# Optimization experiments

Measured on AMD Instinct MI355X. Metric: run time of the kernel, lower is better.

The kernel has to match this reference:

```python
import jax, jax.numpy as jnp
import numpy as np

B, T, D, H, TW = 4, 2048, 2048, 8, 4
DH = D // H


def setup_inputs() -> dict:
    key = jax.random.key(0)
    ks = jax.random.split(key, 16)
    s = lambda k, shape, std: jax.random.normal(k, shape, dtype=jnp.float32) * std
    inp = {
        "x": jax.random.normal(ks[0], (B, T, D), dtype=jnp.float32),
        "segment_pos": jnp.tile(jnp.arange(T, dtype=jnp.int32), (B, 1)),
        # linear_y / linear_x: width -> lru_width, std = 1/sqrt(width)
        "Wy": s(ks[1], (D, D), (1.0 / D) ** 0.5),
        "by": jnp.zeros((D,), jnp.float32),
        "Wx": s(ks[2], (D, D), (1.0 / D) ** 0.5),
        "bx": jnp.zeros((D,), jnp.float32),
        # depthwise causal conv: [temporal_width, lru_width]
        "conv_w": s(ks[3], (TW, D), (1.0 / TW) ** 0.5),
        "conv_b": jnp.zeros((D,), jnp.float32),
        # RG-LRU block-diagonal gates: [H, D/H, D/H]
        "gx_w": s(ks[4], (H, DH, DH), (1.0 / DH) ** 0.5),
        "gx_b": jnp.zeros((H, DH), jnp.float32),
        "ga_w": s(ks[5], (H, DH, DH), (1.0 / DH) ** 0.5),
        "ga_b": jnp.zeros((H, DH), jnp.float32),
        # a_param: softplus(a_param) > 0 controls decay rate
        "a_param": jnp.log(jnp.exp(jax.random.uniform(ks[6], (D,), minval=0.3, maxval=0.9)) - 1.0 + 1e-6),
        # linear_out: lru_width -> width, std = 1/sqrt(lru_width)
        "Wout": s(ks[7], (D, D), (1.0 / D) ** 0.5),
        "bout": jnp.zeros((D,), jnp.float32),
    }
    return inp


def _causal_conv1d(x, w, b, segment_pos):
    # depthwise causal conv over time; contributions from other segments masked
    t = x.shape[1]
    acc = jnp.zeros_like(x)
    for i in range(TW):
        shift = TW - 1 - i  # input at t - shift, weighted by w[i]
        xs = x if shift == 0 else jnp.pad(x, ((0, 0), (shift, 0), (0, 0)))[:, :t]
        mask = (segment_pos >= shift)[..., None].astype(x.dtype)
        acc = acc + xs * mask * w[i]
    return acc + b


def _rg_lru(x, segment_pos, gx_w, gx_b, ga_w, ga_b, a_param):
    b, t, d = x.shape
    xr = x.reshape(b, t, H, DH)
    gate_x = jax.nn.sigmoid(jnp.einsum("bthi,hij->bthj", xr, gx_w) + gx_b).reshape(b, t, d)
    gate_a = jax.nn.sigmoid(jnp.einsum("bthi,hij->bthj", xr, ga_w) + ga_b).reshape(b, t, d)
    log_a = -8.0 * gate_a * jax.nn.softplus(a_param)  # [B,T,D]
    a = jnp.exp(log_a)
    reset = (segment_pos == 0)[..., None]  # [B,T,1]
    multiplier = jnp.sqrt(jnp.maximum(1.0 - jnp.exp(2.0 * log_a), 0.0))
    multiplier = jnp.where(reset, 1.0, multiplier)
    normed = x * gate_x * multiplier
    a_scan = jnp.where(reset, 0.0, a)

    def step(h, inputs):
        a_t, x_t = inputs
        h = a_t * h + x_t
        return h, h

    h0 = jnp.zeros((b, d), x.dtype)
    _, ys = jax.lax.scan(step, h0, (a_scan.transpose(1, 0, 2), normed.transpose(1, 0, 2)))
    return ys.transpose(1, 0, 2)


def reference(x, segment_pos, Wy, by, Wx, bx, conv_w, conv_b, gx_w, gx_b, ga_w, ga_b, a_param, Wout, bout):
    y = jax.nn.gelu(x @ Wy.T + by, approximate=True)
    x_proj = x @ Wx.T + bx
    x_conv = _causal_conv1d(x_proj, conv_w, conv_b, segment_pos)
    x_lru = _rg_lru(x_conv, segment_pos, gx_w, gx_b, ga_w, ga_b, a_param)
    out = (x_lru * y) @ Wout.T + bout
    return out
```

## Files before the change

kernel.cpp:

```cpp
#include <hip/hip_runtime.h>
#include <cstdint>
#include <cstddef>

typedef __bf16 bf16;
typedef __bf16 bf16x8 __attribute__((ext_vector_type(8)));
typedef float f32x4 __attribute__((ext_vector_type(4)));

#define BDIM 4
#define TDIM 2048
#define DDIM 2048
#define HDIM 8
#define DHD 256
#define MTOT 8192
#define NCHUNK 64
#define LCHUNK 32

__device__ __forceinline__ void stage16(const bf16* g, bf16* l) {
  __builtin_amdgcn_global_load_lds(
      (const __attribute__((address_space(1))) void*)g,
      (__attribute__((address_space(3))) void*)l, 16, 0, 0);
}

#define BARX() __builtin_amdgcn_s_barrier()
#define SCHB() __builtin_amdgcn_sched_barrier(0)
#define WAITVM(N) asm volatile("s_waitcnt vmcnt(" #N ")")

__device__ __forceinline__ float sigmoid_f(float x) {
  return __fdividef(1.f, 1.f + __expf(-x));
}
__device__ __forceinline__ float gelu_tanh(float v) {
  float u = 0.7978845608028654f * (v + 0.044715f * v * v * v);
  u = fminf(fmaxf(u, -15.f), 15.f);
  float t = __expf(2.f * u);
  return 0.5f * v * (1.f + __fdividef(t - 1.f, t + 1.f));
}
__device__ __forceinline__ float softplus_f(float x) {
  return __logf(1.f + __expf(x));
}

__global__ __launch_bounds__(256) void f2b(const float* __restrict__ src,
                                           bf16* __restrict__ dst) {
  size_t i = ((size_t)blockIdx.x * 256 + threadIdx.x) * 8;
  const float4 a = *(const float4*)(src + i);
  const float4 b = *(const float4*)(src + i + 4);
  bf16x8 r;
  r[0] = (bf16)a.x; r[1] = (bf16)a.y; r[2] = (bf16)a.z; r[3] = (bf16)a.w;
  r[4] = (bf16)b.x; r[5] = (bf16)b.y; r[6] = (bf16)b.z; r[7] = (bf16)b.w;
  *(bf16x8*)(dst + i) = r;
}

template <typename TO, int EPI>
__global__ __launch_bounds__(512, 2) void gemm256(
    const bf16* __restrict__ A, const bf16* __restrict__ Bm,
    const float* __restrict__ bias, TO* __restrict__ C,
    int K, int lda, int ldb, int ldc) {
  const int gx = gridDim.x, gy = gridDim.y;
  const int nwg = gx * gy;
  const int did = blockIdx.x + gx * blockIdx.y;
  const int cpx = nwg >> 3;
  const int lid = (did & 7) * cpx + (did >> 3);
  const int n0 = (lid % gx) * 256;
  const int m0 = (lid / gx) * 256;

  __shared__ bf16 sA0[256 * 64];
  __shared__ bf16 sA1[256 * 64];
  __shared__ bf16 sB0[256 * 64];
  __shared__ bf16 sB1[256 * 64];
  const int tid = threadIdx.x;
  const int lane = tid & 63;
  const int wid = tid >> 6;
  const int wr = wid >> 2;
  const int wc = wid & 3;
  const int quad = lane >> 4;
  const int l15 = lane & 15;

  const int sr = tid >> 3;
  const int ks8 = ((tid & 7) ^ (sr & 7)) << 3;
  const bf16* Ag = A + (size_t)(m0 + sr) * lda + ks8;
  const bf16* Bg = Bm + (size_t)(n0 + sr) * ldb + ks8;

  const int swz0 = ((quad) ^ (l15 & 7)) << 3;
  const int swz1 = ((4 + quad) ^ (l15 & 7)) << 3;

  f32x4 acc[8][4];
#pragma unroll
  for (int i = 0; i < 8; ++i)
#pragma unroll
    for (int j = 0; j < 4; ++j)
#pragma unroll
      for (int r = 0; r < 4; ++r) acc[i][j][r] = 0.f;

  const int NT = K >> 6;

#define STG_A(ARR, H, TK)                                                     \
  do {                                                                        \
    _Pragma("unroll") for (int j_ = 0; j_ < 2; ++j_) {                        \
      const int c_ = (H) * 2 + j_;                                            \
      stage16(Ag + (size_t)(c_ * 64) * lda + (size_t)(TK) * 64,               \
              &ARR[(c_ * 64 + wid * 8) * 64]);                                \
    }                                                                         \
  } while (0)
#define STG_B(ARR, H, TK)                                                     \
  do {                                                                        \
    _Pragma("unroll") for (int j_ = 0; j_ < 2; ++j_) {                        \
      const int c_ = (H) * 2 + j_;                                            \
      stage16(Bg + (size_t)(c_ * 64) * ldb + (size_t)(TK) * 64,               \
              &ARR[(c_ * 64 + wid * 8) * 64]);                                \
    }                                                                         \
  } while (0)

  bf16x8 aq0[4][2], aq1[4][2], b0[2][2], b1[2][2];

#define RDA(DST, MH, ARR)                                                     \
  do {                                                                        \
    _Pragma("unroll") for (int mi_ = 0; mi_ < 4; ++mi_) {                     \
      const int arow_ = wr * 128 + (MH) * 64 + mi_ * 16 + l15;                \
      DST[mi_][0] = *(const bf16x8*)(&ARR[arow_ * 64] + swz0);                \
      DST[mi_][1] = *(const bf16x8*)(&ARR[arow_ * 64] + swz1);                \
    }                                                                         \
  } while (0)
#define RDB(DST, NH, ARR)                                                     \
  do {                                                                        \
    _Pragma("unroll") for (int ni_ = 0; ni_ < 2; ++ni_) {                     \
      const int brow_ = wc * 64 + (NH) * 32 + ni_ * 16 + l15;                 \
      DST[ni_][0] = *(const bf16x8*)(&ARR[brow_ * 64] + swz0);                \
      DST[ni_][1] = *(const bf16x8*)(&ARR[brow_ * 64] + swz1);                \
    }                                                                         \
  } while (0)
#define MFMAQ(MH, NH, AA, BB)                                                 \
  do {                                                                        \
    __builtin_amdgcn_s_setprio(1);                                            \
    _Pragma("unroll") for (int mi_ = 0; mi_ < 4; ++mi_)                       \
        _Pragma("unroll") for (int ni_ = 0; ni_ < 2; ++ni_) {                 \
      acc[(MH)*4 + mi_][(NH)*2 + ni_] = __builtin_amdgcn_mfma_f32_16x16x32_bf16( \
          AA[mi_][0], BB[ni_][0], acc[(MH)*4 + mi_][(NH)*2 + ni_], 0, 0, 0);  \
      acc[(MH)*4 + mi_][(NH)*2 + ni_] = __builtin_amdgcn_mfma_f32_16x16x32_bf16( \
          AA[mi_][1], BB[ni_][1], acc[(MH)*4 + mi_][(NH)*2 + ni_], 0, 0, 0);  \
    }                                                                         \
    __builtin_amdgcn_s_setprio(0);                                            \
  } while (0)

#define TILE(SAs, SBs, SAo, SBo, T)                                           \
  do {                                                                        \
    const int tn_ = ((T) + 1 < NT) ? (T) + 1 : NT - 1;                        \
    const int tnn_ = ((T) + 2 < NT) ? (T) + 2 : NT - 1;                       \
                                                                     \
    WAITVM(4);                                                                \
    SCHB();                                                                   \
    STG_B(SBo, 1, tn_);                                                       \
    RDB(b1, 1, SBs);                                                          \
    MFMAQ(0, 0, aq0, b0);                                                     \
    BARX();                                                                   \
                                                                     \
    STG_A(SAo, 1, tn_);                                                       \
    RDA(aq1, 1, SAs);                                                         \
    MFMAQ(0, 1, aq0, b1);                                                     \
    BARX();                                                                   \
                                                                     \
    STG_B(SBs, 0, tnn_);                                                      \
    MFMAQ(1, 0, aq1, b0);                                                     \
    BARX();                                                                   \
                                                                     \
    WAITVM(6);                                                                \
    SCHB();                                                                   \
    STG_A(SAs, 0, tnn_);                                                      \
    RDA(aq0, 0, SAo);                                                         \
    RDB(b0, 0, SBo);                                                          \
    MFMAQ(1, 1, aq1, b1);                                                     \
    BARX();                                                                   \
  } while (0)

  STG_B(sB0, 0, 0); STG_A(sA0, 0, 0);
  STG_B(sB0, 1, 0); STG_A(sA0, 1, 0);
  STG_B(sB1, 0, 1); STG_A(sA1, 0, 1);
  WAITVM(8);
  SCHB();
  BARX();
  RDA(aq0, 0, sA0);
  RDB(b0, 0, sB0);

  for (int t = 0; t < NT; t += 2) {
    TILE(sA0, sB0, sA1, sB1, t);
    TILE(sA1, sB1, sA0, sB0, t + 1);
  }
  WAITVM(0);

#undef STG_A
#undef STG_B
#undef RDA
#undef RDB
#undef MFMAQ
#undef TILE

  float bv[4];
#pragma unroll
  for (int nn = 0; nn < 4; ++nn) bv[nn] = bias[n0 + wc * 64 + nn * 16 + l15];
#pragma unroll
  for (int mm = 0; mm < 8; ++mm) {
#pragma unroll
    for (int r = 0; r < 4; ++r) {
      const int m = m0 + wr * 128 + mm * 16 + quad * 4 + r;
      TO* Crow = C + (size_t)m * ldc + n0 + wc * 64 + l15;
#pragma unroll
      for (int nn = 0; nn < 4; ++nn) {
        float v = acc[mm][nn][r] + bv[nn];
        if (EPI == 1) v = gelu_tanh(v);
        Crow[nn * 16] = (TO)v;
      }
    }
  }
}

__global__ __launch_bounds__(256) void gate_gemm(
    const bf16* __restrict__ xconv,
    const bf16* __restrict__ gxT, const bf16* __restrict__ gaT,
    bf16* __restrict__ gxr, bf16* __restrict__ gar) {
  const int h = blockIdx.z >> 1;
  const int g = blockIdx.z & 1;
  const bf16* A = xconv + h * DHD;
  const bf16* Bm = (g ? gaT : gxT) + (size_t)h * DHD * DHD;
  bf16* C = (g ? gar : gxr) + h * DHD;
  const int n0 = blockIdx.x * 128;
  const int m0 = blockIdx.y * 128;
  __shared__ bf16 As[128 * 32];
  __shared__ bf16 Bs[128 * 32];
  const int tid = threadIdx.x;
  const int lane = tid & 63;
  const int wid = tid >> 6;
  const int waveM = wid >> 1, waveN = wid & 1;
  const int quad = lane >> 4;
  const int l15 = lane & 15;
  const int srow = lane >> 2;
  const int scol = (lane & 3) * 8;

  f32x4 acc[4][4];
#pragma unroll
  for (int i = 0; i < 4; ++i)
#pragma unroll
    for (int j = 0; j < 4; ++j)
#pragma unroll
      for (int r = 0; r < 4; ++r) acc[i][j][r] = 0.f;

  for (int k0 = 0; k0 < DHD; k0 += 32) {
    if (k0) __syncthreads();
#pragma unroll
    for (int cc = 0; cc < 2; ++cc) {
      const int q = wid * 2 + cc;
      const int row = q * 16 + srow;
      stage16(A + (size_t)(m0 + row) * DDIM + k0 + scol, As + q * 512);
      stage16(Bm + (size_t)(n0 + row) * DHD + k0 + scol, Bs + q * 512);
    }
    __syncthreads();
    bf16x8 af[4], bfr[4];
#pragma unroll
    for (int i = 0; i < 4; ++i) {
      af[i]  = *(const bf16x8*)&As[(waveM * 64 + i * 16 + l15) * 32 + quad * 8];
      bfr[i] = *(const bf16x8*)&Bs[(waveN * 64 + i * 16 + l15) * 32 + quad * 8];
    }
#pragma unroll
    for (int i = 0; i < 4; ++i)
#pragma unroll
      for (int j = 0; j < 4; ++j)
        acc[i][j] = __builtin_amdgcn_mfma_f32_16x16x32_bf16(af[i], bfr[j], acc[i][j], 0, 0, 0);
  }

#pragma unroll
  for (int j = 0; j < 4; ++j) {
    const int n = n0 + waveN * 64 + j * 16 + l15;
#pragma unroll
    for (int i = 0; i < 4; ++i) {
#pragma unroll
      for (int r = 0; r < 4; ++r) {
        const int m = m0 + waveM * 64 + i * 16 + quad * 4 + r;
        C[(size_t)m * DDIM + n] = (bf16)acc[i][j][r];
      }
    }
  }
}

__global__ __launch_bounds__(256) void conv_kernel(
    const bf16* __restrict__ xp, const float* __restrict__ cw,
    const float* __restrict__ cb, const int* __restrict__ segp,
    bf16* __restrict__ xc) {
  int v = blockIdx.x * 256 + threadIdx.x;
  int dv = v & (DDIM / 8 - 1);
  int m = v >> 8;
  int d0 = dv * 8;
  int t = m & (TDIM - 1);
  int sp = segp[m];
  float acc[8];
#pragma unroll
  for (int j = 0; j < 8; ++j) acc[j] = cb[d0 + j];
#pragma unroll
  for (int i = 0; i < 4; ++i) {
    int shift = 3 - i;
    if (t >= shift && sp >= shift) {
      bf16x8 xv = *(const bf16x8*)&xp[(size_t)(m - shift) * DDIM + d0];
#pragma unroll
      for (int j = 0; j < 8; ++j) acc[j] = fmaf((float)xv[j], cw[i * DDIM + d0 + j], acc[j]);
    }
  }
  bf16x8 o;
#pragma unroll
  for (int j = 0; j < 8; ++j) o[j] = (bf16)acc[j];
  *(bf16x8*)&xc[(size_t)m * DDIM + d0] = o;
}

__global__ __launch_bounds__(256) void transpose_gates(
    const float* __restrict__ gxw, const float* __restrict__ gaw,
    bf16* __restrict__ gxT, bf16* __restrict__ gaT) {
  __shared__ bf16 tile[32][33];
  int zz = blockIdx.z;
  int h = zz >> 1;
  const float* src = (zz & 1) ? gaw : gxw;
  bf16* dst = (zz & 1) ? gaT : gxT;
  int j0 = blockIdx.x * 32;
  int i0 = blockIdx.y * 32;
  int r = threadIdx.x >> 5;
  int c = threadIdx.x & 31;
  for (int rr = r; rr < 32; rr += 8)
    tile[rr][c] = (bf16)src[(size_t)(h * DHD + i0 + rr) * DHD + j0 + c];
  __syncthreads();
  for (int rr = r; rr < 32; rr += 8)
    dst[(size_t)(h * DHD + j0 + rr) * DHD + i0 + c] = tile[c][rr];
}

__device__ __forceinline__ void lru_elem(float pgx, float pga, float xc,
                                         float spv, bool reset,
                                         float& a, float& nr) {
  const float gx = sigmoid_f(pgx);
  const float ga = sigmoid_f(pga);
  const float la = -8.f * ga * spv;
  a = reset ? 0.f : __expf(la);
  const float mult = reset ? 1.f : sqrtf(fmaxf(1.f - __expf(2.f * la), 0.f));
  nr = xc * gx * mult;
}

__global__ __launch_bounds__(256) void scan_phase1(
    const bf16* __restrict__ gxr, const bf16* __restrict__ gar,
    const bf16* __restrict__ xconv,
    const float* __restrict__ gxb, const float* __restrict__ gab,
    const float* __restrict__ apar, const int* __restrict__ segp,
    float* __restrict__ chA, float* __restrict__ chH) {
  int idx = blockIdx.x * 256 + threadIdx.x;
  int d = idx & (DDIM - 1);
  int c = (idx >> 11) & (NCHUNK - 1);
  int b = idx >> 17;
  const float gxbv = gxb[d], gabv = gab[d];
  const float spv = softplus_f(apar[d]);
  const int mrow = b * TDIM + c * LCHUNK;
  size_t base = (size_t)mrow * DDIM + d;
  float A = 1.f, hh = 0.f;
  for (int i = 0; i < LCHUNK; ++i) {
    size_t o = base + (size_t)i * DDIM;
    float a, nr;
    lru_elem((float)gxr[o] + gxbv, (float)gar[o] + gabv, (float)xconv[o],
             spv, segp[mrow + i] == 0, a, nr);
    hh = fmaf(a, hh, nr);
    A *= a;
  }
  int ci = (b * NCHUNK + c) * DDIM + d;
  chA[ci] = A;
  chH[ci] = hh;
}

__global__ __launch_bounds__(256) void scan_phase2(
    const float* __restrict__ chA, const float* __restrict__ chH,
    float* __restrict__ hst) {
  int idx = blockIdx.x * 256 + threadIdx.x;
  int d = idx & (DDIM - 1);
  int b = idx >> 11;
  float s = 0.f;
  for (int c = 0; c < NCHUNK; ++c) {
    int ci = (b * NCHUNK + c) * DDIM + d;
    hst[ci] = s;
    s = fmaf(chA[ci], s, chH[ci]);
  }
}

__global__ __launch_bounds__(256) void scan_phase3(
    const bf16* __restrict__ gxr, const bf16* __restrict__ gar,
    const bf16* __restrict__ xconv,
    const float* __restrict__ gxb, const float* __restrict__ gab,
    const float* __restrict__ apar, const int* __restrict__ segp,
    const float* __restrict__ hst, bf16* __restrict__ yz) {
  int idx = blockIdx.x * 256 + threadIdx.x;
  int d = idx & (DDIM - 1);
  int c = (idx >> 11) & (NCHUNK - 1);
  int b = idx >> 17;
  const float gxbv = gxb[d], gabv = gab[d];
  const float spv = softplus_f(apar[d]);
  const int mrow = b * TDIM + c * LCHUNK;
  size_t base = (size_t)mrow * DDIM + d;
  float hh = hst[(b * NCHUNK + c) * DDIM + d];
  for (int i = 0; i < LCHUNK; ++i) {
    size_t o = base + (size_t)i * DDIM;
    float a, nr;
    lru_elem((float)gxr[o] + gxbv, (float)gar[o] + gabv, (float)xconv[o],
             spv, segp[mrow + i] == 0, a, nr);
    hh = fmaf(a, hh, nr);
    yz[o] = (bf16)(hh * (float)yz[o]);
  }
}

extern "C" void kernel_launch(void* const* d_in, const int* in_sizes, int n_in,
                              void* d_out, int out_size, void* d_ws, size_t ws_size,
                              hipStream_t stream) {
  const float* x    = (const float*)d_in[0];
  const int*   segp = (const int*)d_in[1];
  const float* Wy   = (const float*)d_in[2];
  const float* by   = (const float*)d_in[3];
  const float* Wx   = (const float*)d_in[4];
  const float* bx   = (const float*)d_in[5];
  const float* cw   = (const float*)d_in[6];
  const float* cb   = (const float*)d_in[7];
  const float* gxw  = (const float*)d_in[8];
  const float* gxb  = (const float*)d_in[9];
  const float* gaw  = (const float*)d_in[10];
  const float* gab  = (const float*)d_in[11];
  const float* apar = (const float*)d_in[12];
  const float* Wout = (const float*)d_in[13];
  const float* bout = (const float*)d_in[14];

  const size_t MD = (size_t)MTOT * DDIM;
  const size_t WD = (size_t)DDIM * DDIM;
  bf16* xb    = (bf16*)d_out;
  bf16* xproj = (bf16*)((char*)d_out + MD * 2);
  bf16* xconv = xb;
  bf16* gxr   = xproj;

  char* ws = (char*)d_ws;
  bf16*  gar = (bf16*)ws;
  bf16*  W1  = (bf16*)(ws + MD * 2);
  bf16*  WB1 = (bf16*)(ws + 2 * MD * 2);
  bf16*  WB2 = (bf16*)(ws + 2 * MD * 2 + WD * 2);
  char*  tail = ws + 2 * MD * 2 + 2 * WD * 2;
  const size_t GW = (size_t)HDIM * DHD * DHD * 2;
  const size_t CH = (size_t)BDIM * NCHUNK * DDIM * 4;
  bf16*  gxT = (bf16*)tail;
  bf16*  gaT = (bf16*)(tail + GW);
  float* chA = (float*)(tail + 2 * GW);
  float* chH = (float*)(tail + 2 * GW + CH);
  float* hst = (float*)(tail + 2 * GW + 2 * CH);

  dim3 blk(256);
  f2b<<<dim3(MD / 2048), blk, 0, stream>>>(x, xb);
  f2b<<<dim3(WD / 2048), blk, 0, stream>>>(Wx, WB1);
  f2b<<<dim3(WD / 2048), blk, 0, stream>>>(Wy, WB2);
  transpose_gates<<<dim3(8, 8, 16), blk, 0, stream>>>(gxw, gaw, gxT, gaT);

  gemm256<bf16, 0><<<dim3(8, 32), dim3(512), 0, stream>>>(xb, WB1, bx, xproj, DDIM, DDIM, DDIM, DDIM);
  gemm256<bf16, 1><<<dim3(8, 32), dim3(512), 0, stream>>>(xb, WB2, by, W1, DDIM, DDIM, DDIM, DDIM);

  conv_kernel<<<dim3(MTOT * (DDIM / 8) / 256), blk, 0, stream>>>(xproj, cw, cb, segp, xconv);

  gate_gemm<<<dim3(2, 64, 16), blk, 0, stream>>>(xconv, gxT, gaT, gxr, gar);

  scan_phase1<<<dim3(BDIM * NCHUNK * DDIM / 256), blk, 0, stream>>>(
      gxr, gar, xconv, gxb, gab, apar, segp, chA, chH);
  scan_phase2<<<dim3(BDIM * DDIM / 256), blk, 0, stream>>>(chA, chH, hst);
  scan_phase3<<<dim3(BDIM * NCHUNK * DDIM / 256), blk, 0, stream>>>(
      gxr, gar, xconv, gxb, gab, apar, segp, hst, W1);

  f2b<<<dim3(WD / 2048), blk, 0, stream>>>(Wout, WB1);
  gemm256<float, 0><<<dim3(8, 32), dim3(512), 0, stream>>>(W1, WB1, bout, (float*)d_out, DDIM, DDIM, DDIM, DDIM);
}
```

Baseline: 410.2 us.

## Add batched 128-tile GEMM for input projections and vectorize scan kernels

Adds a 128x128-tile GEMM kernel that computes the x and y input projections in a single launch, using blockIdx.z to select the weight, bias and output, and remaps workgroups for locality. The 256-tile kernel stays in use for the output projection, and its final-iteration LDS prefetch is now skipped. The scan phase-1 and phase-3 kernels each process 8 channels per thread with 16-byte vector loads and stores instead of scalar bf16 accesses. The goals are to cut launches, improve wave occupancy on the projection GEMMs, and raise memory efficiency in the scan. The cost is smaller tiles with less reuse per tile and more registers per thread in the scan.

```diff
diff --git a/kernel.cpp b/kernel.cpp
--- a/kernel.cpp
+++ b/kernel.cpp
@@ -163,9 +163,11 @@
                                                                      \
     WAITVM(6);                                                                \
     SCHB();                                                                   \
+    if (T + 1 < NT) {                                                         \
+      RDA(aq0, 0, SAo);                                                       \
+      RDB(b0, 0, SBo);                                                        \
+    }                                                                         \
     STG_A(SAs, 0, tnn_);                                                      \
-    RDA(aq0, 0, SAo);                                                         \
-    RDB(b0, 0, SBo);                                                          \
     MFMAQ(1, 1, aq1, b1);                                                     \
     BARX();                                                                   \
   } while (0)
@@ -200,6 +202,157 @@
 #pragma unroll
     for (int r = 0; r < 4; ++r) {
       const int m = m0 + wr * 128 + mm * 16 + quad * 4 + r;
+      TO* Crow = C + (size_t)m * ldc + n0 + wc * 64 + l15;
+#pragma unroll
+      for (int nn = 0; nn < 4; ++nn) {
+        float v = acc[mm][nn][r] + bv[nn];
+        if (EPI == 1) v = gelu_tanh(v);
+        Crow[nn * 16] = (TO)v;
+      }
+    }
+  }
+}
+
+template <typename TO>
+__global__ __launch_bounds__(256, 2) void gemm128(
+    const bf16* __restrict__ A,
+    const bf16* __restrict__ B0m, const bf16* __restrict__ B1m,
+    const float* __restrict__ bias0, const float* __restrict__ bias1,
+    TO* __restrict__ C0, TO* __restrict__ C1, int epi1,
+    int K, int lda, int ldb, int ldc) {
+  const bf16* Bm = blockIdx.z ? B1m : B0m;
+  const float* bias = blockIdx.z ? bias1 : bias0;
+  TO* C = blockIdx.z ? C1 : C0;
+  const int EPI = blockIdx.z ? epi1 : 0;
+
+  const int gx = gridDim.x, gy = gridDim.y;
+  const int nwg = gx * gy;
+  const int did = blockIdx.x + gx * blockIdx.y;
+  const int cpx = nwg >> 3;
+  const int lid = (did & 7) * cpx + (did >> 3);
+  const int n0 = (lid % gx) * 128;
+  const int m0 = (lid / gx) * 128;
+
+  __shared__ bf16 sA0[128 * 64];
+  __shared__ bf16 sA1[128 * 64];
+  __shared__ bf16 sB0[128 * 64];
+  __shared__ bf16 sB1[128 * 64];
+  const int tid = threadIdx.x;
+  const int lane = tid & 63;
+  const int wid = tid >> 6;
+  const int wr = wid >> 1;
+  const int wc = wid & 1;
+  const int quad = lane >> 4;
+  const int l15 = lane & 15;
+
+  const int sr = tid >> 3;
+  const int ks8 = ((tid & 7) ^ (sr & 7)) << 3;
+  const bf16* Ag = A + (size_t)(m0 + sr) * lda + ks8;
+  const bf16* Bg = Bm + (size_t)(n0 + sr) * ldb + ks8;
+
+  const int swz0 = ((quad) ^ (l15 & 7)) << 3;
+  const int swz1 = ((4 + quad) ^ (l15 & 7)) << 3;
+
+  f32x4 acc[4][4];
+#pragma unroll
+  for (int i = 0; i < 4; ++i)
+#pragma unroll
+    for (int j = 0; j < 4; ++j)
+#pragma unroll
+      for (int r = 0; r < 4; ++r) acc[i][j][r] = 0.f;
+
+  const int NT = K >> 6;
+
+#define STG_A(ARR, TK)                                                        \
+  do {                                                                        \
+    _Pragma("unroll") for (int c_ = 0; c_ < 4; ++c_)                          \
+        stage16(Ag + (size_t)(c_ * 32) * lda + (size_t)(TK) * 64,             \
+                &ARR[(c_ * 32 + wid * 8) * 64]);                              \
+  } while (0)
+#define STG_B(ARR, TK)                                                        \
+  do {                                                                        \
+    _Pragma("unroll") for (int c_ = 0; c_ < 4; ++c_)                          \
+        stage16(Bg + (size_t)(c_ * 32) * ldb + (size_t)(TK) * 64,             \
+                &ARR[(c_ * 32 + wid * 8) * 64]);                              \
+  } while (0)
+
+  bf16x8 af[4][2], b0[2][2], b1[2][2];
+
+#define RDA(ARR)                                                              \
+  do {                                                                        \
+    _Pragma("unroll") for (int mi_ = 0; mi_ < 4; ++mi_) {                     \
+      const int arow_ = wr * 64 + mi_ * 16 + l15;                             \
+      af[mi_][0] = *(const bf16x8*)(&ARR[arow_ * 64] + swz0);                 \
+      af[mi_][1] = *(const bf16x8*)(&ARR[arow_ * 64] + swz1);                 \
+    }                                                                         \
+  } while (0)
+#define RDB(DST, NH, ARR)                                                     \
+  do {                                                                        \
+    _Pragma("unroll") for (int ni_ = 0; ni_ < 2; ++ni_) {                     \
+      const int brow_ = wc * 64 + (NH) * 32 + ni_ * 16 + l15;                 \
+      DST[ni_][0] = *(const bf16x8*)(&ARR[brow_ * 64] + swz0);                \
+      DST[ni_][1] = *(const bf16x8*)(&ARR[brow_ * 64] + swz1);                \
+    }                                                                         \
+  } while (0)
+#define MFMAQ(NH, BB)                                                         \
+  do {                                                                        \
+    __builtin_amdgcn_s_setprio(1);                                            \
+    _Pragma("unroll") for (int mi_ = 0; mi_ < 4; ++mi_)                       \
+        _Pragma("unroll") for (int ni_ = 0; ni_ < 2; ++ni_) {                 \
+      acc[mi_][(NH)*2 + ni_] = __builtin_amdgcn_mfma_f32_16x16x32_bf16(       \
+          af[mi_][0], BB[ni_][0], acc[mi_][(NH)*2 + ni_], 0, 0, 0);           \
+      acc[mi_][(NH)*2 + ni_] = __builtin_amdgcn_mfma_f32_16x16x32_bf16(       \
+          af[mi_][1], BB[ni_][1], acc[mi_][(NH)*2 + ni_], 0, 0, 0);           \
+    }                                                                         \
+    __builtin_amdgcn_s_setprio(0);                                            \
+  } while (0)
+
+#define TILE(SAs, SBs, SAo, SBo, T)                                           \
+  do {                                                                        \
+    const int tn_ = ((T) + 1 < NT) ? (T) + 1 : NT - 1;                        \
+    const int tnn_ = ((T) + 2 < NT) ? (T) + 2 : NT - 1;                       \
+                                                                     \
+    RDA(SAs);                                                                 \
+    RDB(b0, 0, SBs);                                                          \
+    STG_B(SBo, tn_);                                                          \
+    MFMAQ(0, b0);                                                             \
+    BARX();                                                                   \
+                                                                     \
+    RDB(b1, 1, SBs);                                                          \
+    STG_A(SAs, tnn_);                                                         \
+    MFMAQ(1, b1);                                                             \
+    WAITVM(4);                                                                \
+    BARX();                                                                   \
+  } while (0)
+
+  const int t1 = (NT > 1) ? 1 : 0;
+  STG_B(sB0, 0); STG_A(sA0, 0);
+  STG_B(sB1, t1); STG_A(sA1, t1);
+  WAITVM(4);
+  SCHB();
+  BARX();
+
+  for (int t = 0; t < NT; t += 2) {
+    TILE(sA0, sB0, sA1, sB1, t);
+    TILE(sA1, sB1, sA0, sB0, t + 1);
+  }
+  WAITVM(0);
+
+#undef STG_A
+#undef STG_B
+#undef RDA
+#undef RDB
+#undef MFMAQ
+#undef TILE
+
+  float bv[4];
+#pragma unroll
+  for (int nn = 0; nn < 4; ++nn) bv[nn] = bias[n0 + wc * 64 + nn * 16 + l15];
+#pragma unroll
+  for (int mm = 0; mm < 4; ++mm) {
+#pragma unroll
+    for (int r = 0; r < 4; ++r) {
+      const int m = m0 + wr * 64 + mm * 16 + quad * 4 + r;
       TO* Crow = C + (size_t)m * ldc + n0 + wc * 64 + l15;
 #pragma unroll
       for (int nn = 0; nn < 4; ++nn) {
@@ -343,25 +496,45 @@
     const float* __restrict__ apar, const int* __restrict__ segp,
     float* __restrict__ chA, float* __restrict__ chH) {
   int idx = blockIdx.x * 256 + threadIdx.x;
-  int d = idx & (DDIM - 1);
-  int c = (idx >> 11) & (NCHUNK - 1);
-  int b = idx >> 17;
-  const float gxbv = gxb[d], gabv = gab[d];
-  const float spv = softplus_f(apar[d]);
+  int dv = idx & (DDIM / 8 - 1);
+  int c = (idx >> 8) & (NCHUNK - 1);
+  int b = idx >> 14;
+  int d0 = dv * 8;
+  float gxbv[8], gabv[8], spv[8];
+  const float4 gx0 = *(const float4*)(gxb + d0), gx1 = *(const float4*)(gxb + d0 + 4);
+  const float4 ga0 = *(const float4*)(gab + d0), ga1 = *(const float4*)(gab + d0 + 4);
+  const float4 ap0 = *(const float4*)(apar + d0), ap1 = *(const float4*)(apar + d0 + 4);
+  gxbv[0]=gx0.x;gxbv[1]=gx0.y;gxbv[2]=gx0.z;gxbv[3]=gx0.w;
+  gxbv[4]=gx1.x;gxbv[5]=gx1.y;gxbv[6]=gx1.z;gxbv[7]=gx1.w;
+  gabv[0]=ga0.x;gabv[1]=ga0.y;gabv[2]=ga0.z;gabv[3]=ga0.w;
+  gabv[4]=ga1.x;gabv[5]=ga1.y;gabv[6]=ga1.z;gabv[7]=ga1.w;
+  spv[0]=softplus_f(ap0.x);spv[1]=softplus_f(ap0.y);spv[2]=softplus_f(ap0.z);spv[3]=softplus_f(ap0.w);
+  spv[4]=softplus_f(ap1.x);spv[5]=softplus_f(ap1.y);spv[6]=softplus_f(ap1.z);spv[7]=softplus_f(ap1.w);
   const int mrow = b * TDIM + c * LCHUNK;
-  size_t base = (size_t)mrow * DDIM + d;
-  float A = 1.f, hh = 0.f;
+  size_t base = (size_t)mrow * DDIM + d0;
+  float A[8], hh[8];
+#pragma unroll
+  for (int j = 0; j < 8; ++j) { A[j] = 1.f; hh[j] = 0.f; }
   for (int i = 0; i < LCHUNK; ++i) {
     size_t o = base + (size_t)i * DDIM;
-    float a, nr;
-    lru_elem((float)gxr[o] + gxbv, (float)gar[o] + gabv, (float)xconv[o],
-             spv, segp[mrow + i] == 0, a, nr);
-    hh = fmaf(a, hh, nr);
-    A *= a;
-  }
-  int ci = (b * NCHUNK + c) * DDIM + d;
-  chA[ci] = A;
-  chH[ci] = hh;
+    bf16x8 g1 = *(const bf16x8*)&gxr[o];
+    bf16x8 g2 = *(const bf16x8*)&gar[o];
+    bf16x8 xv = *(const bf16x8*)&xconv[o];
+    bool rst = (segp[mrow + i] == 0);
+#pragma unroll
+    for (int j = 0; j < 8; ++j) {
+      float a, nr;
+      lru_elem((float)g1[j] + gxbv[j], (float)g2[j] + gabv[j], (float)xv[j],
+               spv[j], rst, a, nr);
+      hh[j] = fmaf(a, hh[j], nr);
+      A[j] *= a;
+    }
+  }
+  size_t ci = (size_t)(b * NCHUNK + c) * DDIM + d0;
+  *(f32x4*)&chA[ci]     = f32x4{A[0], A[1], A[2], A[3]};
+  *(f32x4*)&chA[ci + 4] = f32x4{A[4], A[5], A[6], A[7]};
+  *(f32x4*)&chH[ci]     = f32x4{hh[0], hh[1], hh[2], hh[3]};
+  *(f32x4*)&chH[ci + 4] = f32x4{hh[4], hh[5], hh[6], hh[7]};
 }
 
 __global__ __launch_bounds__(256) void scan_phase2(
@@ -385,21 +558,44 @@
     const float* __restrict__ apar, const int* __restrict__ segp,
     const float* __restrict__ hst, bf16* __restrict__ yz) {
   int idx = blockIdx.x * 256 + threadIdx.x;
-  int d = idx & (DDIM - 1);
-  int c = (idx >> 11) & (NCHUNK - 1);
-  int b = idx >> 17;
-  const float gxbv = gxb[d], gabv = gab[d];
-  const float spv = softplus_f(apar[d]);
+  int dv = idx & (DDIM / 8 - 1);
+  int c = (idx >> 8) & (NCHUNK - 1);
+  int b = idx >> 14;
+  int d0 = dv * 8;
+  float gxbv[8], gabv[8], spv[8];
+  const float4 gx0 = *(const float4*)(gxb + d0), gx1 = *(const float4*)(gxb + d0 + 4);
+  const float4 ga0 = *(const float4*)(gab + d0), ga1 = *(const float4*)(gab + d0 + 4);
+  const float4 ap0 = *(const float4*)(apar + d0), ap1 = *(const float4*)(apar + d0 + 4);
+  gxbv[0]=gx0.x;gxbv[1]=gx0.y;gxbv[2]=gx0.z;gxbv[3]=gx0.w;
+  gxbv[4]=gx1.x;gxbv[5]=gx1.y;gxbv[6]=gx1.z;gxbv[7]=gx1.w;
+  gabv[0]=ga0.x;gabv[1]=ga0.y;gabv[2]=ga0.z;gabv[3]=ga0.w;
+  gabv[4]=ga1.x;gabv[5]=ga1.y;gabv[6]=ga1.z;gabv[7]=ga1.w;
+  spv[0]=softplus_f(ap0.x);spv[1]=softplus_f(ap0.y);spv[2]=softplus_f(ap0.z);spv[3]=softplus_f(ap0.w);
+  spv[4]=softplus_f(ap1.x);spv[5]=softplus_f(ap1.y);spv[6]=softplus_f(ap1.z);spv[7]=softplus_f(ap1.w);
   const int mrow = b * TDIM + c * LCHUNK;
-  size_t base = (size_t)mrow * DDIM + d;
-  float hh = hst[(b * NCHUNK + c) * DDIM + d];
+  size_t base = (size_t)mrow * DDIM + d0;
+  size_t ci = (size_t)(b * NCHUNK + c) * DDIM + d0;
+  float hh[8];
+  const float4 h0 = *(const float4*)(hst + ci), h1 = *(const float4*)(hst + ci + 4);
+  hh[0]=h0.x;hh[1]=h0.y;hh[2]=h0.z;hh[3]=h0.w;
+  hh[4]=h1.x;hh[5]=h1.y;hh[6]=h1.z;hh[7]=h1.w;
   for (int i = 0; i < LCHUNK; ++i) {
     size_t o = base + (size_t)i * DDIM;
-    float a, nr;
-    lru_elem((float)gxr[o] + gxbv, (float)gar[o] + gabv, (float)xconv[o],
-             spv, segp[mrow + i] == 0, a, nr);
-    hh = fmaf(a, hh, nr);
-    yz[o] = (bf16)(hh * (float)yz[o]);
+    bf16x8 g1 = *(const bf16x8*)&gxr[o];
+    bf16x8 g2 = *(const bf16x8*)&gar[o];
+    bf16x8 xv = *(const bf16x8*)&xconv[o];
+    bf16x8 y8 = *(const bf16x8*)&yz[o];
+    bool rst = (segp[mrow + i] == 0);
+    bf16x8 out;
+#pragma unroll
+    for (int j = 0; j < 8; ++j) {
+      float a, nr;
+      lru_elem((float)g1[j] + gxbv[j], (float)g2[j] + gabv[j], (float)xv[j],
+               spv[j], rst, a, nr);
+      hh[j] = fmaf(a, hh[j], nr);
+      out[j] = (bf16)(hh[j] * (float)y8[j]);
+    }
+    *(bf16x8*)&yz[o] = out;
   }
 }
 
@@ -449,19 +645,20 @@
   f2b<<<dim3(WD / 2048), blk, 0, stream>>>(Wy, WB2);
   transpose_gates<<<dim3(8, 8, 16), blk, 0, stream>>>(gxw, gaw, gxT, gaT);
 
-  gemm256<bf16, 0><<<dim3(8, 32), dim3(512), 0, stream>>>(xb, WB1, bx, xproj, DDIM, DDIM, DDIM, DDIM);
-  gemm256<bf16, 1><<<dim3(8, 32), dim3(512), 0, stream>>>(xb, WB2, by, W1, DDIM, DDIM, DDIM, DDIM);
+  gemm128<bf16><<<dim3(16, 64, 2), blk, 0, stream>>>(
+      xb, WB1, WB2, bx, by, xproj, W1, 1, DDIM, DDIM, DDIM, DDIM);
 
   conv_kernel<<<dim3(MTOT * (DDIM / 8) / 256), blk, 0, stream>>>(xproj, cw, cb, segp, xconv);
 
   gate_gemm<<<dim3(2, 64, 16), blk, 0, stream>>>(xconv, gxT, gaT, gxr, gar);
 
-  scan_phase1<<<dim3(BDIM * NCHUNK * DDIM / 256), blk, 0, stream>>>(
+  scan_phase1<<<dim3(BDIM * NCHUNK * (DDIM / 8) / 256), blk, 0, stream>>>(
       gxr, gar, xconv, gxb, gab, apar, segp, chA, chH);
   scan_phase2<<<dim3(BDIM * DDIM / 256), blk, 0, stream>>>(chA, chH, hst);
-  scan_phase3<<<dim3(BDIM * NCHUNK * DDIM / 256), blk, 0, stream>>>(
+  scan_phase3<<<dim3(BDIM * NCHUNK * (DDIM / 8) / 256), blk, 0, stream>>>(
       gxr, gar, xconv, gxb, gab, apar, segp, hst, W1);
 
   f2b<<<dim3(WD / 2048), blk, 0, stream>>>(Wout, WB1);
-  gemm256<float, 0><<<dim3(8, 32), dim3(512), 0, stream>>>(W1, WB1, bout, (float*)d_out, DDIM, DDIM, DDIM, DDIM);
-}
+  gemm256<float, 0><<<dim3(8, 32), dim3(512), 0, stream>>>(
+      W1, WB1, bout, (float*)d_out, DDIM, DDIM, DDIM, DDIM);
+}
```

New measurement: 448.0 us. 1.09x slower.
